# Optimization experiments

Hardware: AMD Instinct MI355X
Metric: run time of the kernel (lower is better)

## Reference

```python
import jax, jax.numpy as jnp
import numpy as np

B, T = 256, 512
DX, DZ, DH1, DH2, DDZ, DDX = 100, 100, 10, 10, 20, 20


def _gru_cell(x, h, W_ih, W_hh, b_ih, b_hh):
    # PyTorch GRU cell: gates ordered (r, z, n)
    gi = x @ W_ih.T + b_ih
    gh = h @ W_hh.T + b_hh
    i_r, i_z, i_n = jnp.split(gi, 3, axis=-1)
    h_r, h_z, h_n = jnp.split(gh, 3, axis=-1)
    r = jax.nn.sigmoid(i_r + h_r)
    u = jax.nn.sigmoid(i_z + h_z)
    n = jnp.tanh(i_n + r * h_n)
    return (1.0 - u) * n + u * h


def _mlp(h_in, W1, b1, Wloc, bloc, Wscale, bscale):
    # stoch_trans: relu hidden -> (loc, softplus scale)
    h = jax.nn.relu(h_in @ W1.T + b1)
    return h @ Wloc.T + bloc, jax.nn.softplus(h @ Wscale.T + bscale)


def setup_inputs() -> dict:
    key = jax.random.key(0)
    ks = jax.random.split(key, 22)
    w = lambda k, s: (jax.random.normal(k, s) * 0.1).astype(jnp.float32)
    return dict(
        x=jax.random.normal(ks[0], (B, T, DX), dtype=jnp.float32),
        eps=jax.random.normal(ks[1], (B, T, DZ), dtype=jnp.float32),
        W_ih1=w(ks[2], (3 * DH1, DZ)), W_hh1=w(ks[3], (3 * DH1, DH1)),
        b_ih1=w(ks[4], (3 * DH1,)), b_hh1=w(ks[5], (3 * DH1,)),
        W_ih2=w(ks[6], (3 * DH2, DX)), W_hh2=w(ks[7], (3 * DH2, DH2)),
        b_ih2=w(ks[8], (3 * DH2,)), b_hh2=w(ks[9], (3 * DH2,)),
        dz_W1=w(ks[10], (DDZ, DH1)), dz_b1=w(ks[11], (DDZ,)),
        dz_Wloc=w(ks[12], (DZ, DDZ)), dz_bloc=w(ks[13], (DZ,)),
        dz_Wscale=w(ks[14], (DZ, DDZ)), dz_bscale=w(ks[15], (DZ,)),
        dx_W1=w(ks[16], (DDX, DH1 + DH2)), dx_b1=w(ks[17], (DDX,)),
        dx_Wloc=w(ks[18], (DX, DDX)), dx_bloc=w(ks[19], (DX,)),
        dx_Wscale=w(ks[20], (DX, DDX)), dx_bscale=w(ks[21], (DX,)),
        h1_0=jnp.zeros((DH1,), jnp.float32),
        h2_0=jnp.zeros((DH2,), jnp.float32),
    )


def reference(x, eps, W_ih1, W_hh1, b_ih1, b_hh1, W_ih2, W_hh2, b_ih2, b_hh2,
              dz_W1, dz_b1, dz_Wloc, dz_bloc, dz_Wscale, dz_bscale,
              dx_W1, dx_b1, dx_Wloc, dx_bloc, dx_Wscale, dx_bscale,
              h1_0, h2_0):
    batch = x.shape[0]
    # gen_RNN_2 over the whole observation sequence (no z dependence -> one scan)
    h2_init = jnp.broadcast_to(h2_0, (batch, DH2))
    def step2(h, xt):
        hn = _gru_cell(xt, h, W_ih2, W_hh2, b_ih2, b_hh2)
        return hn, hn
    _, h2_seq = jax.lax.scan(step2, h2_init, jnp.swapaxes(x, 0, 1))  # (T, B, DH2)
    # dx at step t uses h2 after t-1 inputs; first step uses h2_0
    h2_shift = jnp.concatenate([h2_init[None], h2_seq[:-1]], axis=0)

    # sequential generative rollout: dz MLP -> reparam sample -> gen_RNN_1 step -> dx MLP
    h1_init = jnp.broadcast_to(h1_0, (batch, DH1))
    def step(h1, inp):
        eps_t, h2_t = inp
        z_loc, z_scale = _mlp(h1, dz_W1, dz_b1, dz_Wloc, dz_bloc, dz_Wscale, dz_bscale)
        z_t = z_loc + z_scale * eps_t  # reparameterized Normal sample
        h1n = _gru_cell(z_t, h1, W_ih1, W_hh1, b_ih1, b_hh1)
        x_loc, x_scale = _mlp(jnp.concatenate([h1n, h2_t], axis=-1),
                              dx_W1, dx_b1, dx_Wloc, dx_bloc, dx_Wscale, dx_bscale)
        return h1n, (z_t, z_loc, z_scale, x_loc, x_scale)
    _, outs = jax.lax.scan(step, h1_init, (jnp.swapaxes(eps, 0, 1), h2_shift))
    z_t, z_loc, z_scale, x_loc, x_scale = (jnp.swapaxes(o, 0, 1) for o in outs)
    # (B, T, 2*DX + 3*DZ)
    return jnp.concatenate([x_loc, x_scale, z_loc, z_scale, z_t], axis=-1)
```

## Files before the change

kernel.cpp:

```cpp
#include <hip/hip_runtime.h>

#define NB   256
#define NT   512
#define DHX  100
#define DHZ  100
#define DOUT 500
#define WIN  8
#define RING 16

__device__ __forceinline__ float sgm(float v) { return 1.f / (1.f + __expf(-v)); }
__device__ __forceinline__ float tnh(float v) {
    v = fminf(fmaxf(v, -15.f), 15.f);
    float e = __expf(2.f * v);
    return (e - 1.f) / (e + 1.f);
}
__device__ __forceinline__ float sftp(float v) {
    return fmaxf(v, 0.f) + __logf(1.f + __expf(-fabsf(v)));
}

__global__ __launch_bounds__(128, 1) void arfssm(
    const float* __restrict__ x, const float* __restrict__ eps,
    const float* __restrict__ W_ih1, const float* __restrict__ W_hh1,
    const float* __restrict__ b_ih1, const float* __restrict__ b_hh1,
    const float* __restrict__ W_ih2, const float* __restrict__ W_hh2,
    const float* __restrict__ b_ih2, const float* __restrict__ b_hh2,
    const float* __restrict__ dz_W1, const float* __restrict__ dz_b1,
    const float* __restrict__ dz_Wloc, const float* __restrict__ dz_bloc,
    const float* __restrict__ dz_Wscale, const float* __restrict__ dz_bscale,
    const float* __restrict__ dx_W1, const float* __restrict__ dx_b1,
    const float* __restrict__ dx_Wloc, const float* __restrict__ dx_bloc,
    const float* __restrict__ dx_Wscale, const float* __restrict__ dx_bscale,
    const float* __restrict__ h1_0, const float* __restrict__ h2_0,
    float* __restrict__ out)
{
    __shared__ __align__(16) float h1d[RING][12];
    __shared__ __align__(16) float xbuf[2][104];
    __shared__ __align__(16) float zbuf[104];
    __shared__ __align__(16) float hdzs[20];
    __shared__ __align__(16) float hdxs[20];
    __shared__ __align__(16) float h2new[12];
    __shared__ __align__(16) float gA[32];
    __shared__ __align__(16) float gB[32];
    __shared__ __align__(16) float gA2[32];
    __shared__ __align__(16) float gB2[32];

    const int tid = threadIdx.x;
    const int b   = blockIdx.x;

    if (tid < 64) {
        const int l = tid;

        float wdz1[10]; float bdz1 = 0.f;
        #pragma unroll
        for (int k = 0; k < 10; ++k) wdz1[k] = 0.f;
        if (l < 20) {
            #pragma unroll
            for (int k = 0; k < 10; ++k) wdz1[k] = dz_W1[l * 10 + k];
            bdz1 = dz_b1[l];
        }
        float wzl1[20], wzs1[20];
        #pragma unroll
        for (int k = 0; k < 20; ++k) { wzl1[k] = dz_Wloc[l * 20 + k]; wzs1[k] = dz_Wscale[l * 20 + k]; }
        const float bzl1 = dz_bloc[l], bzs1 = dz_bscale[l];
        float wzl2[20], wzs2[20]; float bzl2 = 0.f, bzs2 = 0.f;
        #pragma unroll
        for (int k = 0; k < 20; ++k) { wzl2[k] = 0.f; wzs2[k] = 0.f; }
        if (l < 36) {
            const int j2 = l + 64;
            #pragma unroll
            for (int k = 0; k < 20; ++k) { wzl2[k] = dz_Wloc[j2 * 20 + k]; wzs2[k] = dz_Wscale[j2 * 20 + k]; }
            bzl2 = dz_bloc[j2]; bzs2 = dz_bscale[j2];
        }
        const int gi_i = l >> 1, gi_h = l & 1;
        float wA[52]; float bihA = 0.f, bhh1r = 0.f; float whh1r[10];
        #pragma unroll
        for (int k = 0; k < 52; ++k) wA[k] = 0.f;
        #pragma unroll
        for (int k = 0; k < 10; ++k) whh1r[k] = 0.f;
        if (l < 60) {
            const int k0 = gi_h ? 52 : 0;
            const int kn = gi_h ? 48 : 52;
            #pragma unroll
            for (int k = 0; k < 52; ++k) if (k < kn) wA[k] = W_ih1[gi_i * 100 + k0 + k];
            bihA = b_ih1[gi_i];
            if (gi_h == 0) {
                #pragma unroll
                for (int k = 0; k < 10; ++k) whh1r[k] = W_hh1[gi_i * 10 + k];
                bhh1r = b_hh1[gi_i];
            }
        }

        if (l < 10) h1d[0][l] = h1_0[l];
        if (l < 4)  zbuf[100 + l] = 0.f;
        float e1c = eps[(size_t)b * NT * DHZ + l];
        float e2c = 0.f;
        if (l < 36) e2c = eps[(size_t)b * NT * DHZ + 64 + l];

        for (int w = 0; w < 64; ++w) {
            #pragma unroll 2
            for (int i = 0; i < 8; ++i) {
                const int t  = 8 * w + i;
                const int rs = t & (RING - 1);
                const int wsl = (t + 1) & (RING - 1);
                float h1r[10];
                {
                    float4 a = *(const float4*)&h1d[rs][0];
                    float4 c = *(const float4*)&h1d[rs][4];
                    h1r[0]=a.x; h1r[1]=a.y; h1r[2]=a.z; h1r[3]=a.w;
                    h1r[4]=c.x; h1r[5]=c.y; h1r[6]=c.z; h1r[7]=c.w;
                    h1r[8]=h1d[rs][8]; h1r[9]=h1d[rs][9];
                }
                const int tn = (t + 1 < NT) ? (t + 1) : t;
                const float* ern = eps + ((size_t)b * NT + tn) * DHZ;
                float e1n = ern[l];
                float e2n = 0.f;
                if (l < 36) e2n = ern[64 + l];

                if (l < 20) {
                    float v = bdz1;
                    #pragma unroll
                    for (int k = 0; k < 10; ++k) v = fmaf(wdz1[k], h1r[k], v);
                    hdzs[l] = fmaxf(v, 0.f);
                }
                __builtin_amdgcn_wave_barrier();
                float hdzr[20];
                #pragma unroll
                for (int q = 0; q < 5; ++q) {
                    float4 h4 = *(const float4*)&hdzs[4 * q];
                    hdzr[4*q]=h4.x; hdzr[4*q+1]=h4.y; hdzr[4*q+2]=h4.z; hdzr[4*q+3]=h4.w;
                }

                const size_t ob = ((size_t)b * NT + t) * DOUT;
                {
                    float vl = bzl1, vs = bzs1;
                    #pragma unroll
                    for (int k = 0; k < 20; ++k) { vl = fmaf(wzl1[k], hdzr[k], vl); vs = fmaf(wzs1[k], hdzr[k], vs); }
                    float sp = sftp(vs);
                    float zt = fmaf(sp, e1c, vl);
                    zbuf[l] = zt;
                    out[ob + 200 + l] = vl;
                    out[ob + 300 + l] = sp;
                    out[ob + 400 + l] = zt;
                }
                if (l < 36) {
                    float vl = bzl2, vs = bzs2;
                    #pragma unroll
                    for (int k = 0; k < 20; ++k) { vl = fmaf(wzl2[k], hdzr[k], vl); vs = fmaf(wzs2[k], hdzr[k], vs); }
                    float sp = sftp(vs);
                    float zt = fmaf(sp, e2c, vl);
                    zbuf[64 + l] = zt;
                    out[ob + 264 + l] = vl;
                    out[ob + 364 + l] = sp;
                    out[ob + 464 + l] = zt;
                }
                e1c = e1n; e2c = e2n;
                __builtin_amdgcn_wave_barrier();

                if (l < 60) {
                    const float4* z4 = (const float4*)zbuf;
                    const int b4 = gi_h ? 13 : 0;
                    float a0=0.f, a1=0.f, a2=0.f, a3=0.f;
                    #pragma unroll
                    for (int q = 0; q < 13; ++q) {
                        float4 zz = z4[b4 + q];
                        a0 = fmaf(wA[4*q+0], zz.x, a0);
                        a1 = fmaf(wA[4*q+1], zz.y, a1);
                        a2 = fmaf(wA[4*q+2], zz.z, a2);
                        a3 = fmaf(wA[4*q+3], zz.w, a3);
                    }
                    float acc = (a0 + a1) + (a2 + a3);
                    acc += __shfl_xor(acc, 1, 64);
                    if (gi_h == 0) {
                        float gh = bhh1r;
                        #pragma unroll
                        for (int k = 0; k < 10; ++k) gh = fmaf(whh1r[k], h1r[k], gh);
                        gA[gi_i] = acc + bihA;
                        gB[gi_i] = gh;
                    }
                }
                __builtin_amdgcn_wave_barrier();

                if (l < 10) {
                    float r = sgm(gA[l] + gB[l]);
                    float u = sgm(gA[l + 10] + gB[l + 10]);
                    float n = tnh(fmaf(r, gB[l + 20], gA[l + 20]));
                    h1d[wsl][l] = (1.f - u) * n + u * h1r[l];
                }
                __builtin_amdgcn_wave_barrier();
            }
            __syncthreads();
        }
        __syncthreads();
    } else {
        const int l = tid - 64;

        float wdx1[20]; float bdx1 = 0.f;
        #pragma unroll
        for (int k = 0; k < 20; ++k) wdx1[k] = 0.f;
        if (l < 20) {
            #pragma unroll
            for (int k = 0; k < 20; ++k) wdx1[k] = dx_W1[l * 20 + k];
            bdx1 = dx_b1[l];
        }
        float wxl1[20], wxs1[20];
        #pragma unroll
        for (int k = 0; k < 20; ++k) { wxl1[k] = dx_Wloc[l * 20 + k]; wxs1[k] = dx_Wscale[l * 20 + k]; }
        const float bxl1 = dx_bloc[l], bxs1 = dx_bscale[l];
        float wxl2[20], wxs2[20]; float bxl2 = 0.f, bxs2 = 0.f;
        #pragma unroll
        for (int k = 0; k < 20; ++k) { wxl2[k] = 0.f; wxs2[k] = 0.f; }
        if (l < 36) {
            const int j2 = l + 64;
            #pragma unroll
            for (int k = 0; k < 20; ++k) { wxl2[k] = dx_Wloc[j2 * 20 + k]; wxs2[k] = dx_Wscale[j2 * 20 + k]; }
            bxl2 = dx_bloc[j2]; bxs2 = dx_bscale[j2];
        }
        const int gi_i = l >> 1, gi_h = l & 1;
        float wB[52]; float bihB = 0.f, bhh2r = 0.f; float whh2r[10];
        #pragma unroll
        for (int k = 0; k < 52; ++k) wB[k] = 0.f;
        #pragma unroll
        for (int k = 0; k < 10; ++k) whh2r[k] = 0.f;
        if (l < 60) {
            const int k0 = gi_h ? 52 : 0;
            const int kn = gi_h ? 48 : 52;
            #pragma unroll
            for (int k = 0; k < 52; ++k) if (k < kn) wB[k] = W_ih2[gi_i * 100 + k0 + k];
            bihB = b_ih2[gi_i];
            if (gi_h == 0) {
                #pragma unroll
                for (int k = 0; k < 10; ++k) whh2r[k] = W_hh2[gi_i * 10 + k];
                bhh2r = b_hh2[gi_i];
            }
        }
        float h2r[10];
        #pragma unroll
        for (int k = 0; k < 10; ++k) h2r[k] = h2_0[k];

        if (l < 4) { xbuf[0][100 + l] = 0.f; xbuf[1][100 + l] = 0.f; }
        float4 vh = make_float4(0.f, 0.f, 0.f, 0.f);
        if (l < 25) {
            const float4* xr0 = (const float4*)(x + (size_t)b * NT * DHX);
            const float4* xr1 = (const float4*)(x + ((size_t)b * NT + 1) * DHX);
            float4 v0 = xr0[l];
            vh = xr1[l];
            *((float4*)&xbuf[0][0] + l) = v0;
        }

        __syncthreads();
        for (int w = 1; w < 65; ++w) {
            #pragma unroll 2
            for (int i = 0; i < 8; ++i) {
                const int t = 8 * (w - 1) + i;

                if (l < 25) *((float4*)&xbuf[(t + 1) & 1][0] + l) = vh;
                {
                    const int tn = (t + 2 < NT) ? (t + 2) : (NT - 1);
                    const float4* xr = (const float4*)(x + ((size_t)b * NT + tn) * DHX);
                    if (l < 25) vh = xr[l];
                }

                const int hs = (t + 1) & (RING - 1);
                if (l < 20) {
                    float4 a = *(const float4*)&h1d[hs][0];
                    float4 c = *(const float4*)&h1d[hs][4];
                    float v = bdx1;
                    v = fmaf(wdx1[0], a.x, v); v = fmaf(wdx1[1], a.y, v);
                    v = fmaf(wdx1[2], a.z, v); v = fmaf(wdx1[3], a.w, v);
                    v = fmaf(wdx1[4], c.x, v); v = fmaf(wdx1[5], c.y, v);
                    v = fmaf(wdx1[6], c.z, v); v = fmaf(wdx1[7], c.w, v);
                    v = fmaf(wdx1[8], h1d[hs][8], v); v = fmaf(wdx1[9], h1d[hs][9], v);
                    #pragma unroll
                    for (int k = 0; k < 10; ++k) v = fmaf(wdx1[10 + k], h2r[k], v);
                    hdxs[l] = fmaxf(v, 0.f);
                }
                __builtin_amdgcn_wave_barrier();
                float hdxr[20];
                #pragma unroll
                for (int q = 0; q < 5; ++q) {
                    float4 h4 = *(const float4*)&hdxs[4 * q];
                    hdxr[4*q]=h4.x; hdxr[4*q+1]=h4.y; hdxr[4*q+2]=h4.z; hdxr[4*q+3]=h4.w;
                }
                const size_t ob = ((size_t)b * NT + t) * DOUT;
                {
                    float vl = bxl1, vs = bxs1;
                    #pragma unroll
                    for (int k = 0; k < 20; ++k) { vl = fmaf(wxl1[k], hdxr[k], vl); vs = fmaf(wxs1[k], hdxr[k], vs); }
                    out[ob + l]       = vl;
                    out[ob + 100 + l] = sftp(vs);
                }
                if (l < 36) {
                    float vl = bxl2, vs = bxs2;
                    #pragma unroll
                    for (int k = 0; k < 20; ++k) { vl = fmaf(wxl2[k], hdxr[k], vl); vs = fmaf(wxs2[k], hdxr[k], vs); }
                    out[ob + 64 + l]  = vl;
                    out[ob + 164 + l] = sftp(vs);
                }
                __builtin_amdgcn_wave_barrier();

                if (l < 60) {
                    const float4* x4 = (const float4*)&xbuf[t & 1][0];
                    const int b4 = gi_h ? 13 : 0;
                    float a0=0.f, a1=0.f, a2=0.f, a3=0.f;
                    #pragma unroll
                    for (int q = 0; q < 13; ++q) {
                        float4 xx = x4[b4 + q];
                        a0 = fmaf(wB[4*q+0], xx.x, a0);
                        a1 = fmaf(wB[4*q+1], xx.y, a1);
                        a2 = fmaf(wB[4*q+2], xx.z, a2);
                        a3 = fmaf(wB[4*q+3], xx.w, a3);
                    }
                    float acc = (a0 + a1) + (a2 + a3);
                    acc += __shfl_xor(acc, 1, 64);
                    if (gi_h == 0) {
                        float gh = bhh2r;
                        #pragma unroll
                        for (int k = 0; k < 10; ++k) gh = fmaf(whh2r[k], h2r[k], gh);
                        gA2[gi_i] = acc + bihB;
                        gB2[gi_i] = gh;
                    }
                }
                __builtin_amdgcn_wave_barrier();
                if (l < 10) {
                    float r = sgm(gA2[l] + gB2[l]);
                    float u = sgm(gA2[l + 10] + gB2[l + 10]);
                    float n = tnh(fmaf(r, gB2[l + 20], gA2[l + 20]));
                    h2new[l] = (1.f - u) * n + u * h2r[l];
                }
                __builtin_amdgcn_wave_barrier();
                {
                    float4 a = *(const float4*)&h2new[0];
                    float4 c = *(const float4*)&h2new[4];
                    h2r[0]=a.x; h2r[1]=a.y; h2r[2]=a.z; h2r[3]=a.w;
                    h2r[4]=c.x; h2r[5]=c.y; h2r[6]=c.z; h2r[7]=c.w;
                    h2r[8]=h2new[8]; h2r[9]=h2new[9];
                }
            }
            __syncthreads();
        }
    }
}

extern "C" void kernel_launch(void* const* d_in, const int* in_sizes, int n_in,
                              void* d_out, int out_size, void* d_ws, size_t ws_size,
                              hipStream_t stream) {
    (void)in_sizes; (void)n_in; (void)out_size; (void)d_ws; (void)ws_size;
    const float* x         = (const float*)d_in[0];
    const float* eps       = (const float*)d_in[1];
    const float* W_ih1     = (const float*)d_in[2];
    const float* W_hh1     = (const float*)d_in[3];
    const float* b_ih1     = (const float*)d_in[4];
    const float* b_hh1     = (const float*)d_in[5];
    const float* W_ih2     = (const float*)d_in[6];
    const float* W_hh2     = (const float*)d_in[7];
    const float* b_ih2     = (const float*)d_in[8];
    const float* b_hh2     = (const float*)d_in[9];
    const float* dz_W1     = (const float*)d_in[10];
    const float* dz_b1     = (const float*)d_in[11];
    const float* dz_Wloc   = (const float*)d_in[12];
    const float* dz_bloc   = (const float*)d_in[13];
    const float* dz_Wscale = (const float*)d_in[14];
    const float* dz_bscale = (const float*)d_in[15];
    const float* dx_W1     = (const float*)d_in[16];
    const float* dx_b1     = (const float*)d_in[17];
    const float* dx_Wloc   = (const float*)d_in[18];
    const float* dx_bloc   = (const float*)d_in[19];
    const float* dx_Wscale = (const float*)d_in[20];
    const float* dx_bscale = (const float*)d_in[21];
    const float* h1_0      = (const float*)d_in[22];
    const float* h2_0      = (const float*)d_in[23];

    arfssm<<<NB, 128, 0, stream>>>(x, eps, W_ih1, W_hh1, b_ih1, b_hh1,
                                   W_ih2, W_hh2, b_ih2, b_hh2,
                                   dz_W1, dz_b1, dz_Wloc, dz_bloc, dz_Wscale, dz_bscale,
                                   dx_W1, dx_b1, dx_Wloc, dx_bloc, dx_Wscale, dx_bscale,
                                   h1_0, h2_0, (float*)d_out);
}
```

Before: 888.9 us.

## Replace LDS exchanges with readlane/shuffle broadcasts in per-step recurrence

Inside each recurrent step, intermediate vectors (MLP hidden activations, GRU gate partial sums, new hidden state) were passed through shared memory with wave barriers. They now move between lanes in registers using readlane broadcasts and __shfl gathers. This removes several LDS round trips and barriers from the serial critical path. It also merges the two output-chunk branches, and the h2 GRU gates are now computed before the dx MLP so the two can overlap. In exchange, all lanes run the redundant work and there are more cross-lane ops and higher register pressure.

```diff
diff --git a/kernel.cpp b/kernel.cpp
--- a/kernel.cpp
+++ b/kernel.cpp
@@ -16,6 +16,9 @@
 }
 __device__ __forceinline__ float sftp(float v) {
     return fmaxf(v, 0.f) + __logf(1.f + __expf(-fabsf(v)));
+}
+__device__ __forceinline__ float rdlane(float v, int k) {
+    return __uint_as_float(__builtin_amdgcn_readlane(__float_as_uint(v), (unsigned)k));
 }
 
 __global__ __launch_bounds__(128, 1) void arfssm(
@@ -36,13 +39,6 @@
     __shared__ __align__(16) float h1d[RING][12];
     __shared__ __align__(16) float xbuf[2][104];
     __shared__ __align__(16) float zbuf[104];
-    __shared__ __align__(16) float hdzs[20];
-    __shared__ __align__(16) float hdxs[20];
-    __shared__ __align__(16) float h2new[12];
-    __shared__ __align__(16) float gA[32];
-    __shared__ __align__(16) float gB[32];
-    __shared__ __align__(16) float gA2[32];
-    __shared__ __align__(16) float gB2[32];
 
     const int tid = threadIdx.x;
     const int b   = blockIdx.x;
@@ -72,121 +68,98 @@
             bzl2 = dz_bloc[j2]; bzs2 = dz_bscale[j2];
         }
         const int gi_i = l >> 1, gi_h = l & 1;
-        float wA[52]; float bihA = 0.f, bhh1r = 0.f; float whh1r[10];
+        float wA[52]; float bih_p = 0.f, bhh_p = 0.f; float whh_p[10];
         #pragma unroll
         for (int k = 0; k < 52; ++k) wA[k] = 0.f;
         #pragma unroll
-        for (int k = 0; k < 10; ++k) whh1r[k] = 0.f;
+        for (int k = 0; k < 10; ++k) whh_p[k] = 0.f;
         if (l < 60) {
             const int k0 = gi_h ? 52 : 0;
             const int kn = gi_h ? 48 : 52;
             #pragma unroll
             for (int k = 0; k < 52; ++k) if (k < kn) wA[k] = W_ih1[gi_i * 100 + k0 + k];
-            bihA = b_ih1[gi_i];
-            if (gi_h == 0) {
-                #pragma unroll
-                for (int k = 0; k < 10; ++k) whh1r[k] = W_hh1[gi_i * 10 + k];
-                bhh1r = b_hh1[gi_i];
-            }
-        }
-
-        if (l < 10) h1d[0][l] = h1_0[l];
-        if (l < 4)  zbuf[100 + l] = 0.f;
+            bih_p = b_ih1[gi_i];
+            bhh_p = b_hh1[gi_i];
+            #pragma unroll
+            for (int k = 0; k < 10; ++k) whh_p[k] = W_hh1[gi_i * 10 + k];
+        }
+
+        float hs[10];
+        #pragma unroll
+        for (int k = 0; k < 10; ++k) hs[k] = h1_0[k];
+        float h1own = (l < 10) ? h1_0[l] : 0.f;
+        if (l < 4) zbuf[100 + l] = 0.f;
         float e1c = eps[(size_t)b * NT * DHZ + l];
-        float e2c = 0.f;
-        if (l < 36) e2c = eps[(size_t)b * NT * DHZ + 64 + l];
+        float e2c = (l < 36) ? eps[(size_t)b * NT * DHZ + 64 + l] : 0.f;
 
         for (int w = 0; w < 64; ++w) {
             #pragma unroll 2
             for (int i = 0; i < 8; ++i) {
-                const int t  = 8 * w + i;
-                const int rs = t & (RING - 1);
+                const int t   = 8 * w + i;
                 const int wsl = (t + 1) & (RING - 1);
-                float h1r[10];
-                {
-                    float4 a = *(const float4*)&h1d[rs][0];
-                    float4 c = *(const float4*)&h1d[rs][4];
-                    h1r[0]=a.x; h1r[1]=a.y; h1r[2]=a.z; h1r[3]=a.w;
-                    h1r[4]=c.x; h1r[5]=c.y; h1r[6]=c.z; h1r[7]=c.w;
-                    h1r[8]=h1d[rs][8]; h1r[9]=h1d[rs][9];
-                }
+
+                float hv = bdz1;
+                #pragma unroll
+                for (int k = 0; k < 10; ++k) hv = fmaf(wdz1[k], hs[k], hv);
+                hv = fmaxf(hv, 0.f);
+                float hd[20];
+                #pragma unroll
+                for (int k = 0; k < 20; ++k) hd[k] = rdlane(hv, k);
+
                 const int tn = (t + 1 < NT) ? (t + 1) : t;
                 const float* ern = eps + ((size_t)b * NT + tn) * DHZ;
                 float e1n = ern[l];
-                float e2n = 0.f;
-                if (l < 36) e2n = ern[64 + l];
-
-                if (l < 20) {
-                    float v = bdz1;
-                    #pragma unroll
-                    for (int k = 0; k < 10; ++k) v = fmaf(wdz1[k], h1r[k], v);
-                    hdzs[l] = fmaxf(v, 0.f);
-                }
+                float e2n = (l < 36) ? ern[64 + l] : 0.f;
+
+                float vl1 = bzl1, vs1 = bzs1, vl2 = bzl2, vs2 = bzs2;
+                #pragma unroll
+                for (int k = 0; k < 20; ++k) {
+                    vl1 = fmaf(wzl1[k], hd[k], vl1); vs1 = fmaf(wzs1[k], hd[k], vs1);
+                    vl2 = fmaf(wzl2[k], hd[k], vl2); vs2 = fmaf(wzs2[k], hd[k], vs2);
+                }
+                float sp1 = sftp(vs1), sp2 = sftp(vs2);
+                float zt1 = fmaf(sp1, e1c, vl1);
+                float zt2 = fmaf(sp2, e2c, vl2);
+                zbuf[l] = zt1;
+                if (l < 36) zbuf[64 + l] = zt2;
                 __builtin_amdgcn_wave_barrier();
-                float hdzr[20];
-                #pragma unroll
-                for (int q = 0; q < 5; ++q) {
-                    float4 h4 = *(const float4*)&hdzs[4 * q];
-                    hdzr[4*q]=h4.x; hdzr[4*q+1]=h4.y; hdzr[4*q+2]=h4.z; hdzr[4*q+3]=h4.w;
-                }
 
                 const size_t ob = ((size_t)b * NT + t) * DOUT;
-                {
-                    float vl = bzl1, vs = bzs1;
-                    #pragma unroll
-                    for (int k = 0; k < 20; ++k) { vl = fmaf(wzl1[k], hdzr[k], vl); vs = fmaf(wzs1[k], hdzr[k], vs); }
-                    float sp = sftp(vs);
-                    float zt = fmaf(sp, e1c, vl);
-                    zbuf[l] = zt;
-                    out[ob + 200 + l] = vl;
-                    out[ob + 300 + l] = sp;
-                    out[ob + 400 + l] = zt;
-                }
-                if (l < 36) {
-                    float vl = bzl2, vs = bzs2;
-                    #pragma unroll
-                    for (int k = 0; k < 20; ++k) { vl = fmaf(wzl2[k], hdzr[k], vl); vs = fmaf(wzs2[k], hdzr[k], vs); }
-                    float sp = sftp(vs);
-                    float zt = fmaf(sp, e2c, vl);
-                    zbuf[64 + l] = zt;
-                    out[ob + 264 + l] = vl;
-                    out[ob + 364 + l] = sp;
-                    out[ob + 464 + l] = zt;
-                }
+                out[ob + 200 + l] = vl1; out[ob + 300 + l] = sp1; out[ob + 400 + l] = zt1;
+                if (l < 36) { out[ob + 264 + l] = vl2; out[ob + 364 + l] = sp2; out[ob + 464 + l] = zt2; }
                 e1c = e1n; e2c = e2n;
-                __builtin_amdgcn_wave_barrier();
-
-                if (l < 60) {
-                    const float4* z4 = (const float4*)zbuf;
-                    const int b4 = gi_h ? 13 : 0;
-                    float a0=0.f, a1=0.f, a2=0.f, a3=0.f;
-                    #pragma unroll
-                    for (int q = 0; q < 13; ++q) {
-                        float4 zz = z4[b4 + q];
-                        a0 = fmaf(wA[4*q+0], zz.x, a0);
-                        a1 = fmaf(wA[4*q+1], zz.y, a1);
-                        a2 = fmaf(wA[4*q+2], zz.z, a2);
-                        a3 = fmaf(wA[4*q+3], zz.w, a3);
-                    }
-                    float acc = (a0 + a1) + (a2 + a3);
-                    acc += __shfl_xor(acc, 1, 64);
-                    if (gi_h == 0) {
-                        float gh = bhh1r;
-                        #pragma unroll
-                        for (int k = 0; k < 10; ++k) gh = fmaf(whh1r[k], h1r[k], gh);
-                        gA[gi_i] = acc + bihA;
-                        gB[gi_i] = gh;
-                    }
-                }
-                __builtin_amdgcn_wave_barrier();
-
-                if (l < 10) {
-                    float r = sgm(gA[l] + gB[l]);
-                    float u = sgm(gA[l + 10] + gB[l + 10]);
-                    float n = tnh(fmaf(r, gB[l + 20], gA[l + 20]));
-                    h1d[wsl][l] = (1.f - u) * n + u * h1r[l];
-                }
-                __builtin_amdgcn_wave_barrier();
+
+                const float4* z4 = (const float4*)zbuf;
+                const int b4 = gi_h ? 13 : 0;
+                float a0 = 0.f, a1 = 0.f, a2 = 0.f, a3 = 0.f;
+                #pragma unroll
+                for (int q = 0; q < 13; ++q) {
+                    float4 zz = z4[b4 + q];
+                    a0 = fmaf(wA[4*q+0], zz.x, a0);
+                    a1 = fmaf(wA[4*q+1], zz.y, a1);
+                    a2 = fmaf(wA[4*q+2], zz.z, a2);
+                    a3 = fmaf(wA[4*q+3], zz.w, a3);
+                }
+                float acc = (a0 + a1) + (a2 + a3);
+                acc += __shfl_xor(acc, 1, 64);
+                float gh = bhh_p;
+                #pragma unroll
+                for (int k = 0; k < 10; ++k) gh = fmaf(whh_p[k], hs[k], gh);
+                float gih  = acc + bih_p;
+                float gsum = gih + gh;
+
+                float s_r  = __shfl(gsum, 2 * l,      64);
+                float s_u  = __shfl(gsum, 2 * l + 20, 64);
+                float g_in = __shfl(gih,  2 * l + 40, 64);
+                float g_hn = __shfl(gh,   2 * l + 40, 64);
+                float r = sgm(s_r), u = sgm(s_u);
+                float n = tnh(fmaf(r, g_hn, g_in));
+                float h1n_v = (1.f - u) * n + u * h1own;
+
+                if (l < 10) h1d[wsl][l] = h1n_v;
+                #pragma unroll
+                for (int k = 0; k < 10; ++k) hs[k] = rdlane(h1n_v, k);
+                h1own = h1n_v;
             }
             __syncthreads();
         }
@@ -216,26 +189,26 @@
             bxl2 = dx_bloc[j2]; bxs2 = dx_bscale[j2];
         }
         const int gi_i = l >> 1, gi_h = l & 1;
-        float wB[52]; float bihB = 0.f, bhh2r = 0.f; float whh2r[10];
+        float wB[52]; float bih_p = 0.f, bhh_p = 0.f; float whh_p[10];
         #pragma unroll
         for (int k = 0; k < 52; ++k) wB[k] = 0.f;
         #pragma unroll
-        for (int k = 0; k < 10; ++k) whh2r[k] = 0.f;
+        for (int k = 0; k < 10; ++k) whh_p[k] = 0.f;
         if (l < 60) {
             const int k0 = gi_h ? 52 : 0;
             const int kn = gi_h ? 48 : 52;
             #pragma unroll
             for (int k = 0; k < 52; ++k) if (k < kn) wB[k] = W_ih2[gi_i * 100 + k0 + k];
-            bihB = b_ih2[gi_i];
-            if (gi_h == 0) {
-                #pragma unroll
-                for (int k = 0; k < 10; ++k) whh2r[k] = W_hh2[gi_i * 10 + k];
-                bhh2r = b_hh2[gi_i];
-            }
-        }
-        float h2r[10];
-        #pragma unroll
-        for (int k = 0; k < 10; ++k) h2r[k] = h2_0[k];
+            bih_p = b_ih2[gi_i];
+            bhh_p = b_hh2[gi_i];
+            #pragma unroll
+            for (int k = 0; k < 10; ++k) whh_p[k] = W_hh2[gi_i * 10 + k];
+        }
+
+        float hs2[10];
+        #pragma unroll
+        for (int k = 0; k < 10; ++k) hs2[k] = h2_0[k];
+        float h2own = (l < 10) ? h2_0[l] : 0.f;
 
         if (l < 4) { xbuf[0][100 + l] = 0.f; xbuf[1][100 + l] = 0.f; }
         float4 vh = make_float4(0.f, 0.f, 0.f, 0.f);
@@ -256,85 +229,67 @@
                 if (l < 25) *((float4*)&xbuf[(t + 1) & 1][0] + l) = vh;
                 {
                     const int tn = (t + 2 < NT) ? (t + 2) : (NT - 1);
-                    const float4* xr = (const float4*)(x + ((size_t)b * NT + tn) * DHX);
-                    if (l < 25) vh = xr[l];
-                }
-
-                const int hs = (t + 1) & (RING - 1);
-                if (l < 20) {
-                    float4 a = *(const float4*)&h1d[hs][0];
-                    float4 c = *(const float4*)&h1d[hs][4];
-                    float v = bdx1;
-                    v = fmaf(wdx1[0], a.x, v); v = fmaf(wdx1[1], a.y, v);
-                    v = fmaf(wdx1[2], a.z, v); v = fmaf(wdx1[3], a.w, v);
-                    v = fmaf(wdx1[4], c.x, v); v = fmaf(wdx1[5], c.y, v);
-                    v = fmaf(wdx1[6], c.z, v); v = fmaf(wdx1[7], c.w, v);
-                    v = fmaf(wdx1[8], h1d[hs][8], v); v = fmaf(wdx1[9], h1d[hs][9], v);
-                    #pragma unroll
-                    for (int k = 0; k < 10; ++k) v = fmaf(wdx1[10 + k], h2r[k], v);
-                    hdxs[l] = fmaxf(v, 0.f);
-                }
-                __builtin_amdgcn_wave_barrier();
-                float hdxr[20];
-                #pragma unroll
-                for (int q = 0; q < 5; ++q) {
-                    float4 h4 = *(const float4*)&hdxs[4 * q];
-                    hdxr[4*q]=h4.x; hdxr[4*q+1]=h4.y; hdxr[4*q+2]=h4.z; hdxr[4*q+3]=h4.w;
+                    if (l < 25) vh = ((const float4*)(x + ((size_t)b * NT + tn) * DHX))[l];
+                }
+
+                const int hsl = (t + 1) & (RING - 1);
+                float4 ha = *(const float4*)&h1d[hsl][0];
+                float4 hb = *(const float4*)&h1d[hsl][4];
+                float h8 = h1d[hsl][8], h9 = h1d[hsl][9];
+
+                const float4* x4 = (const float4*)&xbuf[t & 1][0];
+                const int b4 = gi_h ? 13 : 0;
+                float a0 = 0.f, a1 = 0.f, a2 = 0.f, a3 = 0.f;
+                #pragma unroll
+                for (int q = 0; q < 13; ++q) {
+                    float4 xx = x4[b4 + q];
+                    a0 = fmaf(wB[4*q+0], xx.x, a0);
+                    a1 = fmaf(wB[4*q+1], xx.y, a1);
+                    a2 = fmaf(wB[4*q+2], xx.z, a2);
+                    a3 = fmaf(wB[4*q+3], xx.w, a3);
+                }
+                float acc = (a0 + a1) + (a2 + a3);
+                acc += __shfl_xor(acc, 1, 64);
+                float gh = bhh_p;
+                #pragma unroll
+                for (int k = 0; k < 10; ++k) gh = fmaf(whh_p[k], hs2[k], gh);
+                float gih  = acc + bih_p;
+                float gsum = gih + gh;
+                float s_r  = __shfl(gsum, 2 * l,      64);
+                float s_u  = __shfl(gsum, 2 * l + 20, 64);
+                float g_in = __shfl(gih,  2 * l + 40, 64);
+                float g_hn = __shfl(gh,   2 * l + 40, 64);
+
+                float hv = bdx1;
+                hv = fmaf(wdx1[0], ha.x, hv); hv = fmaf(wdx1[1], ha.y, hv);
+                hv = fmaf(wdx1[2], ha.z, hv); hv = fmaf(wdx1[3], ha.w, hv);
+                hv = fmaf(wdx1[4], hb.x, hv); hv = fmaf(wdx1[5], hb.y, hv);
+                hv = fmaf(wdx1[6], hb.z, hv); hv = fmaf(wdx1[7], hb.w, hv);
+                hv = fmaf(wdx1[8], h8, hv);   hv = fmaf(wdx1[9], h9, hv);
+                #pragma unroll
+                for (int k = 0; k < 10; ++k) hv = fmaf(wdx1[10 + k], hs2[k], hv);
+                hv = fmaxf(hv, 0.f);
+                float hx[20];
+                #pragma unroll
+                for (int k = 0; k < 20; ++k) hx[k] = rdlane(hv, k);
+
+                float vl1 = bxl1, vs1 = bxs1, vl2 = bxl2, vs2 = bxs2;
+                #pragma unroll
+                for (int k = 0; k < 20; ++k) {
+                    vl1 = fmaf(wxl1[k], hx[k], vl1); vs1 = fmaf(wxs1[k], hx[k], vs1);
+                    vl2 = fmaf(wxl2[k], hx[k], vl2); vs2 = fmaf(wxs2[k], hx[k], vs2);
                 }
                 const size_t ob = ((size_t)b * NT + t) * DOUT;
-                {
-                    float vl = bxl1, vs = bxs1;
-                    #pragma unroll
-                    for (int k = 0; k < 20; ++k) { vl = fmaf(wxl1[k], hdxr[k], vl); vs = fmaf(wxs1[k], hdxr[k], vs); }
-                    out[ob + l]       = vl;
-                    out[ob + 100 + l] = sftp(vs);
-                }
-                if (l < 36) {
-                    float vl = bxl2, vs = bxs2;
-                    #pragma unroll
-                    for (int k = 0; k < 20; ++k) { vl = fmaf(wxl2[k], hdxr[k], vl); vs = fmaf(wxs2[k], hdxr[k], vs); }
-                    out[ob + 64 + l]  = vl;
-                    out[ob + 164 + l] = sftp(vs);
-                }
-                __builtin_amdgcn_wave_barrier();
-
-                if (l < 60) {
-                    const float4* x4 = (const float4*)&xbuf[t & 1][0];
-                    const int b4 = gi_h ? 13 : 0;
-                    float a0=0.f, a1=0.f, a2=0.f, a3=0.f;
-                    #pragma unroll
-                    for (int q = 0; q < 13; ++q) {
-                        float4 xx = x4[b4 + q];
-                        a0 = fmaf(wB[4*q+0], xx.x, a0);
-                        a1 = fmaf(wB[4*q+1], xx.y, a1);
-                        a2 = fmaf(wB[4*q+2], xx.z, a2);
-                        a3 = fmaf(wB[4*q+3], xx.w, a3);
-                    }
-                    float acc = (a0 + a1) + (a2 + a3);
-                    acc += __shfl_xor(acc, 1, 64);
-                    if (gi_h == 0) {
-                        float gh = bhh2r;
-                        #pragma unroll
-                        for (int k = 0; k < 10; ++k) gh = fmaf(whh2r[k], h2r[k], gh);
-                        gA2[gi_i] = acc + bihB;
-                        gB2[gi_i] = gh;
-                    }
-                }
-                __builtin_amdgcn_wave_barrier();
-                if (l < 10) {
-                    float r = sgm(gA2[l] + gB2[l]);
-                    float u = sgm(gA2[l + 10] + gB2[l + 10]);
-                    float n = tnh(fmaf(r, gB2[l + 20], gA2[l + 20]));
-                    h2new[l] = (1.f - u) * n + u * h2r[l];
-                }
-                __builtin_amdgcn_wave_barrier();
-                {
-                    float4 a = *(const float4*)&h2new[0];
-                    float4 c = *(const float4*)&h2new[4];
-                    h2r[0]=a.x; h2r[1]=a.y; h2r[2]=a.z; h2r[3]=a.w;
-                    h2r[4]=c.x; h2r[5]=c.y; h2r[6]=c.z; h2r[7]=c.w;
-                    h2r[8]=h2new[8]; h2r[9]=h2new[9];
-                }
+                out[ob + l]       = vl1;
+                out[ob + 100 + l] = sftp(vs1);
+                if (l < 36) { out[ob + 64 + l] = vl2; out[ob + 164 + l] = sftp(vs2); }
+
+                float r = sgm(s_r), u = sgm(s_u);
+                float n = tnh(fmaf(r, g_hn, g_in));
+                float h2n_v = (1.f - u) * n + u * h2own;
+                #pragma unroll
+                for (int k = 0; k < 10; ++k) hs2[k] = rdlane(h2n_v, k);
+                h2own = h2n_v;
             }
             __syncthreads();
         }
```

Measured after the change: 776.3 us. 12.7% less time.
